# Kernel tuning notes

Measured on AMD Instinct MI355X. Metric: run time of the kernel, lower is better.

## Reference

```python
import jax, jax.numpy as jnp
import numpy as np

N_NODES, N_EDGES, F_IN, DIM, N_GRAPHS = 50000, 800000, 128, 256, 256


def setup_inputs() -> dict:
    key = jax.random.key(0)
    ks = jax.random.split(key, 6)
    x = jax.random.normal(ks[0], (N_NODES, F_IN), jnp.float32)
    src = jax.random.randint(ks[1], (N_EDGES,), 0, N_NODES, jnp.int32)
    dst = jax.random.randint(ks[2], (N_EDGES,), 0, N_NODES, jnp.int32)
    node2graph = jnp.sort(jax.random.randint(ks[3], (N_NODES,), 0, N_GRAPHS, jnp.int32))
    W1 = jax.random.normal(ks[4], (F_IN, DIM), jnp.float32) * (1.0 / np.sqrt(F_IN))
    b1 = jnp.zeros((DIM,), jnp.float32)
    W2 = jax.random.normal(ks[5], (DIM, DIM), jnp.float32) * (1.0 / np.sqrt(DIM))
    b2 = jnp.zeros((DIM,), jnp.float32)
    return {"x": x, "W1": W1, "b1": b1, "W2": W2, "b2": b2,
            "src": src, "dst": dst, "node2graph": node2graph}


def reference(x, W1, b1, W2, b2, src, dst, node2graph):
    n = x.shape[0]
    ones = jnp.ones(src.shape[0], x.dtype)
    # DGL GraphConv norm='both': symmetric degree normalization, degrees clamped to >= 1
    out_norm = jnp.maximum(jax.ops.segment_sum(ones, src, num_segments=n), 1.0) ** -0.5
    in_norm = jnp.maximum(jax.ops.segment_sum(ones, dst, num_segments=n), 1.0) ** -0.5

    def gcn_layer(h, W, b):
        msg = (h * out_norm[:, None])[src]                      # [E, d] gather
        agg = jax.ops.segment_sum(msg, dst, num_segments=n)     # [N, d] scatter-add
        return (agg * in_norm[:, None]) @ W + b

    h = jax.nn.relu(gcn_layer(x, W1, b1))   # relu on all but last layer
    h = gcn_layer(h, W2, b2)                # last layer: no activation
    # scale: sqrt(dim) / mean node L2 norm (computed on first forward)
    factor = jnp.sqrt(jnp.asarray(DIM, h.dtype)) / jnp.mean(jnp.linalg.norm(h, axis=1))
    h = h * factor
    # SumPooling: per-graph segment sum
    return jax.ops.segment_sum(h, node2graph, num_segments=N_GRAPHS)
```

## Files before the change

### kernel.cpp

```cpp
#include <hip/hip_runtime.h>

#define NODES 50000
#define EDGES 800000
#define FIN 128
#define DIM 256
#define GRAPHS 256
#define PAD_M 50048
#define SCAN_BLOCKS ((NODES + 255) / 256)
#define PRESCALE_BLOCKS (NODES * FIN / 4 / 256)
#define HBLOCKS 256
#define CHUNK (EDGES / HBLOCKS)
#define HALF_N 25000
#define HALF_W 12500

typedef short short8 __attribute__((ext_vector_type(8)));
typedef float f32x4 __attribute__((ext_vector_type(4)));

__device__ __forceinline__ float bf2f(uint u) { return __uint_as_float(u << 16); }
__device__ __forceinline__ ushort f2bf(float f) {
    uint b = __float_as_uint(f);
    return (ushort)((b + 0x7FFF + ((b >> 16) & 1)) >> 16);
}

__global__ __launch_bounds__(256) void hist_kernel(const int* __restrict__ idx,
                                                   uint* __restrict__ histG) {
    __shared__ uint cur[HALF_W];
    int b = blockIdx.x, tid = threadIdx.x;
    int base = b * CHUNK;
    for (int half = 0; half < 2; ++half) {
        for (int j = tid; j < HALF_W; j += 256) cur[j] = 0;
        __syncthreads();
        int lo = half * HALF_N;
        for (int e = base + tid; e < base + CHUNK; e += 256) {
            int local = idx[e] - lo;
            if ((unsigned)local < (unsigned)HALF_N)
                atomicAdd(&cur[local >> 1], 1u << ((local & 1) * 16));
        }
        __syncthreads();
        uint* dstp = histG + (size_t)b * (2 * HALF_W) + half * HALF_W;
        for (int j = tid; j < HALF_W; j += 256) dstp[j] = cur[j];
        __syncthreads();
    }
}

__global__ __launch_bounds__(256) void reduce_hist_kernel(uint* __restrict__ histIn,
                                                          const uint* __restrict__ histOut,
                                                          int* __restrict__ deg_in,
                                                          float* __restrict__ in_norm,
                                                          float* __restrict__ out_norm) {
    int t32 = blockIdx.x * 256 + threadIdx.x;
    if (t32 >= 2 * HALF_W) return;
    uint lo = 0, hi = 0;
#pragma unroll 4
    for (int c = 0; c < HBLOCKS; ++c) {
        size_t a = (size_t)c * (2 * HALF_W) + t32;
        uint u = histIn[a];
        histIn[a] = lo | (hi << 16);
        lo += u & 0xFFFFu;
        hi += u >> 16;
    }
    uint olo = 0, ohi = 0;
#pragma unroll 4
    for (int c = 0; c < HBLOCKS; ++c) {
        uint u = histOut[(size_t)c * (2 * HALF_W) + t32];
        olo += u & 0xFFFFu;
        ohi += u >> 16;
    }
    int n0 = (t32 < HALF_W) ? 2 * t32 : HALF_N + 2 * (t32 - HALF_W);
    deg_in[n0]     = (int)lo;
    deg_in[n0 + 1] = (int)hi;
    in_norm[n0]      = rsqrtf(fmaxf((float)lo, 1.0f));
    in_norm[n0 + 1]  = rsqrtf(fmaxf((float)hi, 1.0f));
    out_norm[n0]     = rsqrtf(fmaxf((float)olo, 1.0f));
    out_norm[n0 + 1] = rsqrtf(fmaxf((float)ohi, 1.0f));
}

__global__ __launch_bounds__(256) void scan_partials(const int* __restrict__ deg_in,
                                                     int* __restrict__ block_sums, int n) {
    __shared__ int red[4];
    int i = blockIdx.x * 256 + threadIdx.x;
    int v = (i < n) ? deg_in[i] : 0;
    int wave = threadIdx.x >> 6, lane = threadIdx.x & 63;
#pragma unroll
    for (int off = 32; off > 0; off >>= 1) v += __shfl_down(v, off);
    if (lane == 0) red[wave] = v;
    __syncthreads();
    if (threadIdx.x == 0) block_sums[blockIdx.x] = red[0] + red[1] + red[2] + red[3];
}

__global__ __launch_bounds__(256) void scan_blocksums(int* __restrict__ block_sums,
                                                      int* __restrict__ row_start,
                                                      float* __restrict__ norm_sum, int nb, int n) {
    __shared__ int s[256];
    int t = threadIdx.x;
    if (t == 0) *norm_sum = 0.0f;
    int v = (t < nb) ? block_sums[t] : 0;
    s[t] = v;
    __syncthreads();
#pragma unroll
    for (int off = 1; off < 256; off <<= 1) {
        int u = (t >= off) ? s[t - off] : 0;
        __syncthreads();
        s[t] += u;
        __syncthreads();
    }
    if (t < nb) block_sums[t] = s[t] - v;
    if (t == nb - 1) row_start[n] = s[t];
}

__global__ __launch_bounds__(256) void scan_final(const int* __restrict__ deg,
                                                  const int* __restrict__ block_sums,
                                                  int* __restrict__ row_start, int n) {
    __shared__ int s[256];
    int t = threadIdx.x;
    int i = blockIdx.x * 256 + t;
    int v = (i < n) ? deg[i] : 0;
    s[t] = v;
    __syncthreads();
#pragma unroll
    for (int off = 1; off < 256; off <<= 1) {
        int u = (t >= off) ? s[t - off] : 0;
        __syncthreads();
        s[t] += u;
        __syncthreads();
    }
    if (i < n) row_start[i] = block_sums[blockIdx.x] + s[t] - v;
}

__global__ __launch_bounds__(256) void scatter_lds_kernel(const int* __restrict__ src,
                                                          const int* __restrict__ dst,
                                                          const uint* __restrict__ histIn,
                                                          const int* __restrict__ row_start,
                                                          int* __restrict__ src_sorted) {
    __shared__ uint cur[HALF_W];
    int b = blockIdx.x, tid = threadIdx.x;
    int base = b * CHUNK;
    for (int half = 0; half < 2; ++half) {
        const uint* offp = histIn + (size_t)b * (2 * HALF_W) + half * HALF_W;
        for (int j = tid; j < HALF_W; j += 256) cur[j] = offp[j];
        __syncthreads();
        int lo = half * HALF_N;
        for (int e = base + tid; e < base + CHUNK; e += 256) {
            int d = dst[e];
            int local = d - lo;
            if ((unsigned)local < (unsigned)HALF_N) {
                int sel = (local & 1) * 16;
                uint old = atomicAdd(&cur[local >> 1], 1u << sel);
                int pos = row_start[d] + (int)((old >> sel) & 0xFFFFu);
                src_sorted[pos] = src[e];
            }
        }
        __syncthreads();
    }
}

__global__ __launch_bounds__(256) void prep_kernel(const float* __restrict__ x,
                                                   const float* __restrict__ out_norm,
                                                   ushort* __restrict__ xs,
                                                   const float* __restrict__ W1,
                                                   ushort* __restrict__ W1T,
                                                   const float* __restrict__ W2,
                                                   ushort* __restrict__ W2T) {
    int b = blockIdx.x;
    if (b < PRESCALE_BLOCKS) {
        int t = b * 256 + threadIdx.x;
        int row = t >> 5;
        float on = out_norm[row];
        float4 v = ((const float4*)x)[t];
        ushort4 o;
        o.x = f2bf(v.x * on); o.y = f2bf(v.y * on);
        o.z = f2bf(v.z * on); o.w = f2bf(v.w * on);
        ((ushort4*)xs)[t] = o;
    } else if (b < PRESCALE_BLOCKS + FIN * DIM / 256) {
        int t = (b - PRESCALE_BLOCKS) * 256 + threadIdx.x;
        int n = t >> 7, k = t & 127;
        W1T[t] = f2bf(W1[(size_t)k * DIM + n]);
    } else {
        int t = (b - PRESCALE_BLOCKS - FIN * DIM / 256) * 256 + threadIdx.x;
        int n = t >> 8, k = t & 255;
        W2T[t] = f2bf(W2[(size_t)k * DIM + n]);
    }
}

template<int D>
__global__ __launch_bounds__(256) void agg_kernel(const ushort* __restrict__ in,
                                                  const int* __restrict__ row_start,
                                                  const int* __restrict__ src_sorted,
                                                  const float* __restrict__ in_norm,
                                                  ushort* __restrict__ out) {
    constexpr int VPL = D / 64;
    constexpr int NU = VPL / 2;
    int wave = threadIdx.x >> 6, lane = threadIdx.x & 63;
    int node = blockIdx.x * 4 + wave;
    if (node >= NODES) return;
    int off = lane * VPL;
    int e0 = row_start[node], e1 = row_start[node + 1];
    float acc[VPL] = {};
    int niter = (e1 - e0 + 7) >> 3;
    for (int it = 0; it < niter; ++it) {
        int eb = e0 + it * 8;
        int idx[8];
#pragma unroll
        for (int j = 0; j < 8; ++j) idx[j] = src_sorted[min(eb + j, e1 - 1)];
        uint u[8][NU];
#pragma unroll
        for (int j = 0; j < 8; ++j) {
            const uint* p = (const uint*)(in + (size_t)idx[j] * D + off);
#pragma unroll
            for (int q = 0; q < NU; ++q) u[j][q] = p[q];
        }
#pragma unroll
        for (int j = 0; j < 8; ++j) {
            uint ok = (eb + j < e1) ? 0xFFFFFFFFu : 0u;
#pragma unroll
            for (int q = 0; q < NU; ++q) {
                uint uu = u[j][q] & ok;
                acc[2*q]   += bf2f(uu & 0xFFFFu);
                acc[2*q+1] += bf2f(uu >> 16);
            }
        }
    }
    float inn = in_norm[node];
    uint* po = (uint*)(out + (size_t)node * D + off);
#pragma unroll
    for (int q = 0; q < NU; ++q) {
        uint lo = f2bf(acc[2*q] * inn);
        uint hi = f2bf(acc[2*q+1] * inn);
        po[q] = lo | (hi << 16);
    }
}

template<int K, int MODE>
__global__ __launch_bounds__(256) void gemm_mfma_kernel(const ushort* __restrict__ A,
                                                        const ushort* __restrict__ WT,
                                                        const float* __restrict__ bias,
                                                        ushort* __restrict__ Cout,
                                                        const float* __restrict__ scale,
                                                        float* __restrict__ norm_sum,
                                                        int M) {
    __shared__ float rowsq[4][64];
    int lane = threadIdx.x & 63, wave = threadIdx.x >> 6;
    int m0 = blockIdx.x * 64, n0 = wave * 64;
    int ll = lane & 15, lh = lane >> 4;
    f32x4 acc[4][4] = {};
    const ushort* Ab = A  + (size_t)(m0 + ll) * K + lh * 8;
    const ushort* Bb = WT + (size_t)(n0 + ll) * K + lh * 8;
#pragma unroll
    for (int k0 = 0; k0 < K; k0 += 32) {
        short8 a[4], b[4];
#pragma unroll
        for (int mi = 0; mi < 4; ++mi) a[mi] = *(const short8*)(Ab + (size_t)mi * 16 * K + k0);
#pragma unroll
        for (int ni = 0; ni < 4; ++ni) b[ni] = *(const short8*)(Bb + (size_t)ni * 16 * K + k0);
#pragma unroll
        for (int mi = 0; mi < 4; ++mi)
#pragma unroll
            for (int ni = 0; ni < 4; ++ni)
                acc[mi][ni] = __builtin_amdgcn_mfma_f32_16x16x32_bf16(a[mi], b[ni], acc[mi][ni], 0, 0, 0);
    }
#pragma unroll
    for (int mi = 0; mi < 4; ++mi) {
#pragma unroll
        for (int r = 0; r < 4; ++r) {
            int row = m0 + mi * 16 + lh * 4 + r;
            float sc = (MODE == 0 && row < M) ? scale[row] : 1.0f;
            float p = 0.0f;
#pragma unroll
            for (int ni = 0; ni < 4; ++ni) {
                int col = n0 + ni * 16 + ll;
                float v = acc[mi][ni][r] + bias[col];
                if (MODE == 0) v = fmaxf(v, 0.0f) * sc;
                else p += v * v;
                if (row < M) Cout[(size_t)row * DIM + col] = f2bf(v);
            }
            if (MODE == 1) {
#pragma unroll
                for (int m = 1; m < 16; m <<= 1) p += __shfl_xor(p, m);
                if (ll == 0) rowsq[wave][mi * 16 + lh * 4 + r] = p;
            }
        }
    }
    if (MODE == 1) {
        __syncthreads();
        if (threadIdx.x < 64) {
            int lr = threadIdx.x;
            float s = rowsq[0][lr] + rowsq[1][lr] + rowsq[2][lr] + rowsq[3][lr];
            float l = (m0 + lr < M) ? sqrtf(s) : 0.0f;
#pragma unroll
            for (int m = 32; m > 0; m >>= 1) l += __shfl_down(l, m);
            if (lr == 0) atomicAdd(norm_sum, l);
        }
    }
}

__global__ __launch_bounds__(256) void pool_kernel(const ushort* __restrict__ h2,
                                                   const int* __restrict__ n2g,
                                                   const float* __restrict__ norm_sum,
                                                   float* __restrict__ out) {
    int g = blockIdx.x, f = threadIdx.x;
    int lo = 0, hi = NODES;
    while (lo < hi) { int mid = (lo + hi) >> 1; if (n2g[mid] < g) lo = mid + 1; else hi = mid; }
    int start = lo;
    hi = NODES;
    while (lo < hi) { int mid = (lo + hi) >> 1; if (n2g[mid] < g + 1) lo = mid + 1; else hi = mid; }
    int end = lo;
    float acc = 0.0f;
    int i = start;
    for (; i + 3 < end; i += 4) {
        acc += (bf2f((uint)h2[(size_t)(i + 0) * DIM + f]) + bf2f((uint)h2[(size_t)(i + 1) * DIM + f]))
             + (bf2f((uint)h2[(size_t)(i + 2) * DIM + f]) + bf2f((uint)h2[(size_t)(i + 3) * DIM + f]));
    }
    for (; i < end; ++i) acc += bf2f((uint)h2[(size_t)i * DIM + f]);
    float factor = 16.0f * (float)NODES / *norm_sum;
    out[(size_t)g * DIM + f] = acc * factor;
}

extern "C" void kernel_launch(void* const* d_in, const int* in_sizes, int n_in,
                              void* d_out, int out_size, void* d_ws, size_t ws_size,
                              hipStream_t stream) {
    const float* x  = (const float*)d_in[0];
    const float* W1 = (const float*)d_in[1];
    const float* b1 = (const float*)d_in[2];
    const float* W2 = (const float*)d_in[3];
    const float* b2 = (const float*)d_in[4];
    const int* src = (const int*)d_in[5];
    const int* dst = (const int*)d_in[6];
    const int* n2g = (const int*)d_in[7];
    float* out = (float*)d_out;

    char* ws = (char*)d_ws;
    size_t off = 0;
    auto alloc = [&](size_t bytes) {
        char* p = ws + off;
        off = (off + bytes + 255) & ~(size_t)255;
        return p;
    };
    uint* histIn    = (uint*)alloc((size_t)HBLOCKS * 2 * HALF_W * 4);
    uint* histOut   = (uint*)alloc((size_t)HBLOCKS * 2 * HALF_W * 4);
    int* deg_in     = (int*)alloc(NODES * 4);
    float* out_norm = (float*)alloc(NODES * 4);
    float* in_norm  = (float*)alloc(NODES * 4);
    int* row_start  = (int*)alloc((NODES + 1) * 4);
    int* src_sorted = (int*)alloc(EDGES * 4);
    int* block_sums = (int*)alloc(SCAN_BLOCKS * 4);
    float* norm_sum = (float*)alloc(4);
    ushort* W1T     = (ushort*)alloc((size_t)DIM * FIN * 2);
    ushort* W2T     = (ushort*)alloc((size_t)DIM * DIM * 2);
    ushort* xs  = (ushort*)alloc((size_t)PAD_M * FIN * 2);
    ushort* A1  = (ushort*)alloc((size_t)PAD_M * FIN * 2);
    ushort* h1s = (ushort*)alloc((size_t)PAD_M * DIM * 2);
    ushort* A2 = xs;
    ushort* h2 = h1s;

    hist_kernel<<<HBLOCKS, 256, 0, stream>>>(dst, histIn);
    hist_kernel<<<HBLOCKS, 256, 0, stream>>>(src, histOut);
    reduce_hist_kernel<<<(2 * HALF_W + 255) / 256, 256, 0, stream>>>(histIn, histOut,
                                                                     deg_in, in_norm, out_norm);
    scan_partials<<<SCAN_BLOCKS, 256, 0, stream>>>(deg_in, block_sums, NODES);
    scan_blocksums<<<1, 256, 0, stream>>>(block_sums, row_start, norm_sum, SCAN_BLOCKS, NODES);
    scan_final<<<SCAN_BLOCKS, 256, 0, stream>>>(deg_in, block_sums, row_start, NODES);
    scatter_lds_kernel<<<HBLOCKS, 256, 0, stream>>>(src, dst, histIn, row_start, src_sorted);

    prep_kernel<<<PRESCALE_BLOCKS + FIN * DIM / 256 + DIM * DIM / 256, 256, 0, stream>>>(
        x, out_norm, xs, W1, W1T, W2, W2T);

    agg_kernel<FIN><<<(NODES + 3) / 4, 256, 0, stream>>>(xs, row_start, src_sorted, in_norm, A1);
    gemm_mfma_kernel<FIN, 0><<<PAD_M / 64, 256, 0, stream>>>(A1, W1T, b1, h1s, out_norm, norm_sum, NODES);

    agg_kernel<DIM><<<(NODES + 3) / 4, 256, 0, stream>>>(h1s, row_start, src_sorted, in_norm, A2);
    gemm_mfma_kernel<DIM, 1><<<PAD_M / 64, 256, 0, stream>>>(A2, W2T, b2, h2, nullptr, norm_sum, NODES);

    pool_kernel<<<GRAPHS, 256, 0, stream>>>(h2, n2g, norm_sum, out);
}
```

Measured before the change: 281.7 us.

## Merge histogram, scan and prep kernels to cut launch count in CSR build

Runs both degree histograms in one launch of 2x blocks, folds the per-block scan partial sums into the histogram reduction (each reduce block covers 512 contiguous nodes), and merges the final scan with the prescale/weight-transpose prep kernel. The scan now processes two nodes per thread, so only 98 blocks are needed. This removes several kernel launches and the serialization gaps between them. The price is more complex block-index dispatch and lower parallelism in the scan part.

```diff
diff --git a/kernel.cpp b/kernel.cpp
--- a/kernel.cpp
+++ b/kernel.cpp
@@ -6,12 +6,12 @@
 #define DIM 256
 #define GRAPHS 256
 #define PAD_M 50048
-#define SCAN_BLOCKS ((NODES + 255) / 256)
 #define PRESCALE_BLOCKS (NODES * FIN / 4 / 256)
 #define HBLOCKS 256
 #define CHUNK (EDGES / HBLOCKS)
 #define HALF_N 25000
 #define HALF_W 12500
+#define RB 98
 
 typedef short short8 __attribute__((ext_vector_type(8)));
 typedef float f32x4 __attribute__((ext_vector_type(4)));
@@ -22,10 +22,14 @@
     return (ushort)((b + 0x7FFF + ((b >> 16) & 1)) >> 16);
 }
 
-__global__ __launch_bounds__(256) void hist_kernel(const int* __restrict__ idx,
-                                                   uint* __restrict__ histG) {
+__global__ __launch_bounds__(256) void hist2_kernel(const int* __restrict__ src,
+                                                    const int* __restrict__ dst,
+                                                    uint* __restrict__ histIn,
+                                                    uint* __restrict__ histOut) {
     __shared__ uint cur[HALF_W];
-    int b = blockIdx.x, tid = threadIdx.x;
+    int b = blockIdx.x & 255, tid = threadIdx.x;
+    const int* idx = (blockIdx.x < HBLOCKS) ? dst : src;
+    uint* histG    = (blockIdx.x < HBLOCKS) ? histIn : histOut;
     int base = b * CHUNK;
     for (int half = 0; half < 2; ++half) {
         for (int j = tid; j < HALF_W; j += 256) cur[j] = 0;
@@ -47,43 +51,40 @@
                                                           const uint* __restrict__ histOut,
                                                           int* __restrict__ deg_in,
                                                           float* __restrict__ in_norm,
-                                                          float* __restrict__ out_norm) {
+                                                          float* __restrict__ out_norm,
+                                                          int* __restrict__ block_sums) {
+    __shared__ int red[4];
     int t32 = blockIdx.x * 256 + threadIdx.x;
-    if (t32 >= 2 * HALF_W) return;
     uint lo = 0, hi = 0;
+    if (t32 < 2 * HALF_W) {
 #pragma unroll 4
-    for (int c = 0; c < HBLOCKS; ++c) {
-        size_t a = (size_t)c * (2 * HALF_W) + t32;
-        uint u = histIn[a];
-        histIn[a] = lo | (hi << 16);
-        lo += u & 0xFFFFu;
-        hi += u >> 16;
-    }
-    uint olo = 0, ohi = 0;
+        for (int c = 0; c < HBLOCKS; ++c) {
+            size_t a = (size_t)c * (2 * HALF_W) + t32;
+            uint u = histIn[a];
+            histIn[a] = lo | (hi << 16);
+            lo += u & 0xFFFFu;
+            hi += u >> 16;
+        }
+        uint olo = 0, ohi = 0;
 #pragma unroll 4
-    for (int c = 0; c < HBLOCKS; ++c) {
-        uint u = histOut[(size_t)c * (2 * HALF_W) + t32];
-        olo += u & 0xFFFFu;
-        ohi += u >> 16;
-    }
-    int n0 = (t32 < HALF_W) ? 2 * t32 : HALF_N + 2 * (t32 - HALF_W);
-    deg_in[n0]     = (int)lo;
-    deg_in[n0 + 1] = (int)hi;
-    in_norm[n0]      = rsqrtf(fmaxf((float)lo, 1.0f));
-    in_norm[n0 + 1]  = rsqrtf(fmaxf((float)hi, 1.0f));
-    out_norm[n0]     = rsqrtf(fmaxf((float)olo, 1.0f));
-    out_norm[n0 + 1] = rsqrtf(fmaxf((float)ohi, 1.0f));
-}
-
-__global__ __launch_bounds__(256) void scan_partials(const int* __restrict__ deg_in,
-                                                     int* __restrict__ block_sums, int n) {
-    __shared__ int red[4];
-    int i = blockIdx.x * 256 + threadIdx.x;
-    int v = (i < n) ? deg_in[i] : 0;
+        for (int c = 0; c < HBLOCKS; ++c) {
+            uint u = histOut[(size_t)c * (2 * HALF_W) + t32];
+            olo += u & 0xFFFFu;
+            ohi += u >> 16;
+        }
+        int n0 = 2 * t32;
+        deg_in[n0]     = (int)lo;
+        deg_in[n0 + 1] = (int)hi;
+        in_norm[n0]      = rsqrtf(fmaxf((float)lo, 1.0f));
+        in_norm[n0 + 1]  = rsqrtf(fmaxf((float)hi, 1.0f));
+        out_norm[n0]     = rsqrtf(fmaxf((float)olo, 1.0f));
+        out_norm[n0 + 1] = rsqrtf(fmaxf((float)ohi, 1.0f));
+    }
+    int s = (int)(lo + hi);
     int wave = threadIdx.x >> 6, lane = threadIdx.x & 63;
 #pragma unroll
-    for (int off = 32; off > 0; off >>= 1) v += __shfl_down(v, off);
-    if (lane == 0) red[wave] = v;
+    for (int off = 32; off > 0; off >>= 1) s += __shfl_down(s, off);
+    if (lane == 0) red[wave] = s;
     __syncthreads();
     if (threadIdx.x == 0) block_sums[blockIdx.x] = red[0] + red[1] + red[2] + red[3];
 }
@@ -108,23 +109,53 @@
     if (t == nb - 1) row_start[n] = s[t];
 }
 
-__global__ __launch_bounds__(256) void scan_final(const int* __restrict__ deg,
-                                                  const int* __restrict__ block_sums,
-                                                  int* __restrict__ row_start, int n) {
+__global__ __launch_bounds__(256) void scanfinal_prep_kernel(const int* __restrict__ deg,
+                                                             const int* __restrict__ block_sums,
+                                                             int* __restrict__ row_start,
+                                                             const float* __restrict__ x,
+                                                             const float* __restrict__ out_norm,
+                                                             ushort* __restrict__ xs,
+                                                             const float* __restrict__ W1,
+                                                             ushort* __restrict__ W1T,
+                                                             const float* __restrict__ W2,
+                                                             ushort* __restrict__ W2T) {
     __shared__ int s[256];
-    int t = threadIdx.x;
-    int i = blockIdx.x * 256 + t;
-    int v = (i < n) ? deg[i] : 0;
-    s[t] = v;
-    __syncthreads();
-#pragma unroll
-    for (int off = 1; off < 256; off <<= 1) {
-        int u = (t >= off) ? s[t - off] : 0;
-        __syncthreads();
-        s[t] += u;
-        __syncthreads();
-    }
-    if (i < n) row_start[i] = block_sums[blockIdx.x] + s[t] - v;
+    int b = blockIdx.x, t = threadIdx.x;
+    if (b < RB) {
+        int i0 = b * 512 + 2 * t;
+        int v0 = (i0 < NODES) ? deg[i0] : 0;
+        int v1 = (i0 + 1 < NODES) ? deg[i0 + 1] : 0;
+        int pair = v0 + v1;
+        s[t] = pair;
+        __syncthreads();
+#pragma unroll
+        for (int off = 1; off < 256; off <<= 1) {
+            int u = (t >= off) ? s[t - off] : 0;
+            __syncthreads();
+            s[t] += u;
+            __syncthreads();
+        }
+        int excl = block_sums[b] + s[t] - pair;
+        if (i0 < NODES) row_start[i0] = excl;
+        if (i0 + 1 < NODES) row_start[i0 + 1] = excl + v0;
+    } else if (b < RB + PRESCALE_BLOCKS) {
+        int i = (b - RB) * 256 + t;
+        int row = i >> 5;
+        float on = out_norm[row];
+        float4 v = ((const float4*)x)[i];
+        ushort4 o;
+        o.x = f2bf(v.x * on); o.y = f2bf(v.y * on);
+        o.z = f2bf(v.z * on); o.w = f2bf(v.w * on);
+        ((ushort4*)xs)[i] = o;
+    } else if (b < RB + PRESCALE_BLOCKS + FIN * DIM / 256) {
+        int i = (b - RB - PRESCALE_BLOCKS) * 256 + t;
+        int n = i >> 7, k = i & 127;
+        W1T[i] = f2bf(W1[(size_t)k * DIM + n]);
+    } else {
+        int i = (b - RB - PRESCALE_BLOCKS - FIN * DIM / 256) * 256 + t;
+        int n = i >> 8, k = i & 255;
+        W2T[i] = f2bf(W2[(size_t)k * DIM + n]);
+    }
 }
 
 __global__ __launch_bounds__(256) void scatter_lds_kernel(const int* __restrict__ src,
@@ -151,34 +182,6 @@
             }
         }
         __syncthreads();
-    }
-}
-
-__global__ __launch_bounds__(256) void prep_kernel(const float* __restrict__ x,
-                                                   const float* __restrict__ out_norm,
-                                                   ushort* __restrict__ xs,
-                                                   const float* __restrict__ W1,
-                                                   ushort* __restrict__ W1T,
-                                                   const float* __restrict__ W2,
-                                                   ushort* __restrict__ W2T) {
-    int b = blockIdx.x;
-    if (b < PRESCALE_BLOCKS) {
-        int t = b * 256 + threadIdx.x;
-        int row = t >> 5;
-        float on = out_norm[row];
-        float4 v = ((const float4*)x)[t];
-        ushort4 o;
-        o.x = f2bf(v.x * on); o.y = f2bf(v.y * on);
-        o.z = f2bf(v.z * on); o.w = f2bf(v.w * on);
-        ((ushort4*)xs)[t] = o;
-    } else if (b < PRESCALE_BLOCKS + FIN * DIM / 256) {
-        int t = (b - PRESCALE_BLOCKS) * 256 + threadIdx.x;
-        int n = t >> 7, k = t & 127;
-        W1T[t] = f2bf(W1[(size_t)k * DIM + n]);
-    } else {
-        int t = (b - PRESCALE_BLOCKS - FIN * DIM / 256) * 256 + threadIdx.x;
-        int n = t >> 8, k = t & 255;
-        W2T[t] = f2bf(W2[(size_t)k * DIM + n]);
     }
 }
 
@@ -342,7 +345,7 @@
     float* in_norm  = (float*)alloc(NODES * 4);
     int* row_start  = (int*)alloc((NODES + 1) * 4);
     int* src_sorted = (int*)alloc(EDGES * 4);
-    int* block_sums = (int*)alloc(SCAN_BLOCKS * 4);
+    int* block_sums = (int*)alloc(RB * 4);
     float* norm_sum = (float*)alloc(4);
     ushort* W1T     = (ushort*)alloc((size_t)DIM * FIN * 2);
     ushort* W2T     = (ushort*)alloc((size_t)DIM * DIM * 2);
@@ -352,17 +355,12 @@
     ushort* A2 = xs;
     ushort* h2 = h1s;
 
-    hist_kernel<<<HBLOCKS, 256, 0, stream>>>(dst, histIn);
-    hist_kernel<<<HBLOCKS, 256, 0, stream>>>(src, histOut);
-    reduce_hist_kernel<<<(2 * HALF_W + 255) / 256, 256, 0, stream>>>(histIn, histOut,
-                                                                     deg_in, in_norm, out_norm);
-    scan_partials<<<SCAN_BLOCKS, 256, 0, stream>>>(deg_in, block_sums, NODES);
-    scan_blocksums<<<1, 256, 0, stream>>>(block_sums, row_start, norm_sum, SCAN_BLOCKS, NODES);
-    scan_final<<<SCAN_BLOCKS, 256, 0, stream>>>(deg_in, block_sums, row_start, NODES);
+    hist2_kernel<<<2 * HBLOCKS, 256, 0, stream>>>(src, dst, histIn, histOut);
+    reduce_hist_kernel<<<RB, 256, 0, stream>>>(histIn, histOut, deg_in, in_norm, out_norm, block_sums);
+    scan_blocksums<<<1, 256, 0, stream>>>(block_sums, row_start, norm_sum, RB, NODES);
+    scanfinal_prep_kernel<<<RB + PRESCALE_BLOCKS + FIN * DIM / 256 + DIM * DIM / 256, 256, 0, stream>>>(
+        deg_in, block_sums, row_start, x, out_norm, xs, W1, W1T, W2, W2T);
     scatter_lds_kernel<<<HBLOCKS, 256, 0, stream>>>(src, dst, histIn, row_start, src_sorted);
-
-    prep_kernel<<<PRESCALE_BLOCKS + FIN * DIM / 256 + DIM * DIM / 256, 256, 0, stream>>>(
-        x, out_norm, xs, W1, W1T, W2, W2T);
 
     agg_kernel<FIN><<<(NODES + 3) / 4, 256, 0, stream>>>(xs, row_start, src_sorted, in_norm, A1);
     gemm_mfma_kernel<FIN, 0><<<PAD_M / 64, 256, 0, stream>>>(A1, W1T, b1, h1s, out_norm, norm_sum, NODES);
```

Measured after the change: 269.0 us. 1.05x faster.
